# Performance work log

Measured on AMD Instinct MI355X. Metric: run time of the kernel, lower is better.

## Reference

```python
import jax, jax.numpy as jnp
import numpy as np

NC, NG, D = 50000, 3000, 64
E_CG, E_GC, E_GG = 3_000_000, 3_000_000, 100_000
KEEP = 0.9  # 1 - drop_out


def _mask(key, n):
    return (jax.random.uniform(key, (n, 1)) < KEEP).astype(jnp.float32) / KEEP


def setup_inputs() -> dict:
    key = jax.random.key(0)
    ks = jax.random.split(key, 20)
    return {
        "c_feat": jax.random.normal(ks[0], (NC, D), jnp.float32),
        "g_feat": jax.random.normal(ks[1], (NG, D), jnp.float32),
        "cj_cell": jax.random.uniform(ks[2], (NC, 1), jnp.float32),
        "ci_cell": jax.random.uniform(ks[3], (NC, 1), jnp.float32),
        "cj_gene": jax.random.uniform(ks[4], (NG, 1), jnp.float32),
        "ci_gene": jax.random.uniform(ks[5], (NG, 1), jnp.float32),
        "cjj_gene": jax.random.uniform(ks[6], (NG, 1), jnp.float32),
        "cii_gene": jax.random.uniform(ks[7], (NG, 1), jnp.float32),
        "mask_exp": _mask(ks[8], NC),
        "mask_rev": _mask(ks[9], NG),
        "mask_gg": _mask(ks[10], NG),
        "src_cg": jax.random.randint(ks[11], (E_CG,), 0, NC, jnp.int32),
        "dst_cg": jax.random.randint(ks[12], (E_CG,), 0, NG, jnp.int32),
        "src_gc": jax.random.randint(ks[13], (E_GC,), 0, NG, jnp.int32),
        "dst_gc": jax.random.randint(ks[14], (E_GC,), 0, NC, jnp.int32),
        "src_gg": jax.random.randint(ks[15], (E_GG,), 0, NG, jnp.int32),
        "dst_gg": jax.random.randint(ks[16], (E_GG,), 0, NG, jnp.int32),
    }


def _light_conv(src_feats, cj, mask, ci, src, dst, n_dst):
    # weighted_feats = src_feats * dropout(cj); copy_u + sum; scale by ci
    wf = src_feats * (cj * mask)                      # [Nsrc, D]
    agg = jax.ops.segment_sum(wf[src], dst, num_segments=n_dst)  # [Ndst, D]
    return agg * ci


def reference(c_feat, g_feat, cj_cell, ci_cell, cj_gene, ci_gene,
              cjj_gene, cii_gene, mask_exp, mask_rev, mask_gg,
              src_cg, dst_cg, src_gc, dst_gc, src_gg, dst_gg):
    alpha1 = 0.5
    # relation 'exp': cell -> gene
    g_exp = _light_conv(c_feat, cj_cell, mask_exp, ci_gene, src_cg, dst_cg, NG)
    # relation 'reverse-exp': gene -> cell (only relation targeting cells)
    c_out = _light_conv(g_feat, cj_gene, mask_rev, ci_cell, src_gc, dst_gc, NC)
    # relation 'co-exp': gene -> gene (uses cjj/cii)
    g_gg = _light_conv(g_feat, cjj_gene, mask_gg, cii_gene, src_gg, dst_gg, NG)
    # aggregate='stack' over gene dst relations, then alpha-weighted combine
    g_out = alpha1 * g_exp + (1.0 - alpha1) * g_gg
    return (c_out, g_out)
```

## Files before the change

### kernel.cpp

```cpp
#include <hip/hip_runtime.h>

#define NC 50000
#define NG 3000
#define D  64

#define NB_CG 750
#define NB_GC 782
#define PBITS 18
#define TILE  4096
#define NPREP 128
#define CAP   4608
#define GG_CAP 128
#define OVF_CAP 262144

__device__ inline unsigned short f2bf(float x) {
    unsigned u = __float_as_uint(x);
    unsigned r = u + 0x7FFFu + ((u >> 16) & 1u);
    return (unsigned short)(r >> 16);
}

__device__ __forceinline__ void acc8(const uint4& q, float f[8]) {
    f[0] += __uint_as_float(q.x << 16); f[1] += __uint_as_float(q.x & 0xFFFF0000u);
    f[2] += __uint_as_float(q.y << 16); f[3] += __uint_as_float(q.y & 0xFFFF0000u);
    f[4] += __uint_as_float(q.z << 16); f[5] += __uint_as_float(q.z & 0xFFFF0000u);
    f[6] += __uint_as_float(q.w << 16); f[7] += __uint_as_float(q.w & 0xFFFF0000u);
}

__device__ inline void row8f(const float* feat, int s, int l8, float f[8]) {
    const float4* row = (const float4*)(feat + (size_t)s * D);
    const float4 a = row[l8];
    const float4 b = row[l8 + 8];
    f[0] = a.x; f[1] = a.y; f[2] = a.z; f[3] = a.w;
    f[4] = b.x; f[5] = b.y; f[6] = b.z; f[7] = b.w;
}


__global__ __launch_bounds__(256) void partition_kernel(
    const int* __restrict__ src_cg, const int* __restrict__ dst_cg, int e_cg, int nt_cg,
    const int* __restrict__ src_gc, const int* __restrict__ dst_gc, int e_gc, int nt_gc,
    const int* __restrict__ src_gg, const int* __restrict__ dst_gg, int e_gg,
    int* __restrict__ cur_cg, int* __restrict__ cur_gc, int* __restrict__ cnt_gg,
    unsigned* __restrict__ bkt_cg, unsigned* __restrict__ bkt_gc, int* __restrict__ bkt_gg,
    int* __restrict__ ovf_cnt, uint2* __restrict__ ovf,
    const float* __restrict__ cj_cell, const float* __restrict__ mask_exp,
    const float* __restrict__ cj_gene, const float* __restrict__ mask_rev,
    const float* __restrict__ cjj_gene, const float* __restrict__ mask_gg,
    float* __restrict__ w_cell, float* __restrict__ w_rev, float* __restrict__ w_gg,
    const float* __restrict__ c_feat, const float* __restrict__ g_feat,
    unsigned short* __restrict__ wc16, unsigned short* __restrict__ wg16,
    unsigned short* __restrict__ wgg16, int do_cvt)
{
    const int tid = threadIdx.x;
    const int NT2 = nt_cg + nt_gc;

    if (blockIdx.x >= NT2 + 64) {
        const int pb = blockIdx.x - NT2 - 64;
        const long long stride = (long long)NPREP * 256;
        for (long long i = (long long)pb * 256 + tid; i < NC; i += stride)
            w_cell[i] = cj_cell[i] * mask_exp[i];
        for (long long i = (long long)pb * 256 + tid; i < NG; i += stride) {
            w_rev[i] = cj_gene[i] * mask_rev[i];
            w_gg[i]  = cjj_gene[i] * mask_gg[i];
        }
        if (do_cvt) {
            const long long total8 = (long long)(NC + NG) * D / 8;
            for (long long t = (long long)pb * 256 + tid; t < total8; t += stride) {
                const long long base = t * 8;
                if (base < (long long)NC * D) {
                    const int s = (int)(base >> 6);
                    const float w = cj_cell[s] * mask_exp[s];
                    const float4 a = ((const float4*)(c_feat + base))[0];
                    const float4 b = ((const float4*)(c_feat + base))[1];
                    unsigned short* dp = wc16 + base;
                    ((ushort4*)dp)[0] = make_ushort4(f2bf(w*a.x), f2bf(w*a.y), f2bf(w*a.z), f2bf(w*a.w));
                    ((ushort4*)dp)[1] = make_ushort4(f2bf(w*b.x), f2bf(w*b.y), f2bf(w*b.z), f2bf(w*b.w));
                } else {
                    const long long gb = base - (long long)NC * D;
                    const int s = (int)(gb >> 6);
                    const float wr = cj_gene[s] * mask_rev[s];
                    const float wg = cjj_gene[s] * mask_gg[s];
                    const float4 a = ((const float4*)(g_feat + gb))[0];
                    const float4 b = ((const float4*)(g_feat + gb))[1];
                    ((ushort4*)(wg16 + gb))[0]  = make_ushort4(f2bf(wr*a.x), f2bf(wr*a.y), f2bf(wr*a.z), f2bf(wr*a.w));
                    ((ushort4*)(wg16 + gb))[1]  = make_ushort4(f2bf(wr*b.x), f2bf(wr*b.y), f2bf(wr*b.z), f2bf(wr*b.w));
                    ((ushort4*)(wgg16 + gb))[0] = make_ushort4(f2bf(wg*a.x), f2bf(wg*a.y), f2bf(wg*a.z), f2bf(wg*a.w));
                    ((ushort4*)(wgg16 + gb))[1] = make_ushort4(f2bf(wg*b.x), f2bf(wg*b.y), f2bf(wg*b.z), f2bf(wg*b.w));
                }
            }
            if (pb == 0) {
                for (int i = tid; i < D; i += 256) {
                    wc16[(size_t)NC * D + i] = 0;
                    wg16[(size_t)NG * D + i] = 0;
                    wgg16[(size_t)NG * D + i] = 0;
                }
            }
        }
        return;
    }

    if (blockIdx.x >= NT2) {
        for (long long e = (long long)(blockIdx.x - NT2) * 256 + tid; e < e_gg;
             e += (long long)64 * 256) {
            const int dd = dst_gg[e];
            const int ss = src_gg[e];
            if ((unsigned)dd >= (unsigned)NG || (unsigned)ss >= (unsigned)NG) continue;
            const int pos = atomicAdd(&cnt_gg[dd], 1);
            if (pos < GG_CAP) bkt_gg[dd * GG_CAP + pos] = ss;
            else {
                const int op = atomicAdd(ovf_cnt, 1);
                if (op >= 0 && op < OVF_CAP)
                    ovf[op] = make_uint2((2u << 30) | (unsigned)ss, (unsigned)dd);
            }
        }
        return;
    }

    const int* src; const int* dst; int ne; int* cur; unsigned* bkt;
    int shift, nbins, t; unsigned rel;
    if (blockIdx.x < nt_cg) { src = src_cg; dst = dst_cg; ne = e_cg; cur = cur_cg; bkt = bkt_cg; shift = 2; nbins = NB_CG; t = blockIdx.x;         rel = 0u; }
    else                    { src = src_gc; dst = dst_gc; ne = e_gc; cur = cur_gc; bkt = bkt_gc; shift = 6; nbins = NB_GC; t = blockIdx.x - nt_cg; rel = 1u; }
    const long long tb = (long long)t * TILE;
    if (tb >= ne) return;
    const int n = (int)((ne - tb) < TILE ? (ne - tb) : TILE);

    __shared__ int th[784];
    __shared__ int toff[784];
    __shared__ int gs[784];
    __shared__ unsigned staged[TILE];
    const unsigned PMASK = (1u << PBITS) - 1u;
    const unsigned DMASK = (1u << shift) - 1u;

    for (int i = tid; i < nbins; i += 256) th[i] = 0;
    __syncthreads();
    #pragma unroll 4
    for (int k = 0; k < TILE / 256; ++k) {
        int i = k * 256 + tid;
        if (i < n) {
            unsigned b = ((unsigned)dst[tb + i]) >> shift;
            if (b < (unsigned)nbins) atomicAdd(&th[b], 1);
        }
    }
    __syncthreads();
    if (tid < 64) {
        int carry = 0;
        for (int c = 0; c < nbins; c += 64) {
            int idx = c + tid;
            int v = (idx < nbins) ? th[idx] : 0;
            int incl = v;
            #pragma unroll
            for (int d = 1; d < 64; d <<= 1) {
                int x = __shfl_up(incl, d);
                if (tid >= d) incl += x;
            }
            if (idx < nbins) {
                toff[idx] = incl - v + carry;
                gs[idx] = v ? atomicAdd(&cur[idx], v) : 0;
            }
            carry += __shfl(incl, 63);
        }
    }
    __syncthreads();
    #pragma unroll 4
    for (int k = 0; k < TILE / 256; ++k) {
        int i = k * 256 + tid;
        if (i < n) {
            unsigned d = (unsigned)dst[tb + i];
            unsigned s = (unsigned)src[tb + i];
            unsigned b = d >> shift;
            if (b < (unsigned)nbins) {
                int p = atomicAdd(&toff[b], 1);
                if (p >= 0 && p < TILE)
                    staged[p] = (b << PBITS) | (s << shift) | (d & DMASK);
            }
        }
    }
    __syncthreads();
    for (int i = tid; i < n; i += 256) {
        const unsigned v = staged[i];
        const unsigned b = v >> PBITS;
        if (b < (unsigned)nbins) {
            const int orig = toff[b] - th[b];
            const int local = gs[b] + (i - orig);
            if (local >= 0 && local < CAP) {
                bkt[(size_t)b * CAP + local] = v & PMASK;
            } else {
                const unsigned s = (v >> shift) & 0xFFFFu;
                const unsigned dd = (b << shift) | (v & DMASK);
                const int op = atomicAdd(ovf_cnt, 1);
                if (op >= 0 && op < OVF_CAP)
                    ovf[op] = make_uint2((rel << 30) | s, dd);
            }
        }
    }
}


template <bool BF16>
__global__ __launch_bounds__(256, 6) void gather3_kernel(
    const unsigned* __restrict__ bkt_cg, const int* __restrict__ cur_cg,
    const unsigned* __restrict__ bkt_gc, const int* __restrict__ cur_gc,
    const void* __restrict__ fc, const void* __restrict__ fg, const void* __restrict__ fgg,
    const float* __restrict__ craw, const float* __restrict__ graw,
    const float* __restrict__ w_cell, const float* __restrict__ w_rev, const float* __restrict__ w_gg,
    const float* __restrict__ ci_gene, const float* __restrict__ cii_gene, const float* __restrict__ ci_cell,
    const int* __restrict__ cnt_gg, const int* __restrict__ bkt_gg,
    const int* __restrict__ ovf_cnt, const uint2* __restrict__ ovf,
    float* __restrict__ g_out, float* __restrict__ c_out)
{
    __shared__ unsigned short sorted[CAP];
    __shared__ int lh[64];
    __shared__ int loff[64];
    __shared__ int lcur[64];

    const bool is_cg = (blockIdx.x < NB_CG);
    const int bin = is_cg ? blockIdx.x : blockIdx.x - NB_CG;
    int n = (is_cg ? cur_cg : cur_gc)[bin];
    n = n > CAP ? CAP : n;
    const long long base = (long long)bin * CAP;
    const unsigned* bkt = is_cg ? bkt_cg : bkt_gc;
    const void* feat = is_cg ? fc : fg;
    const float* wsrc = is_cg ? w_cell : w_rev;
    const int shift = is_cg ? 2 : 6;
    const int DIVv = is_cg ? 4 : 64;
    const int KPC  = is_cg ? 16 : 1;
    const int DUM  = is_cg ? NC : NG;
    const int tid  = threadIdx.x;
    const int lane = tid & 63;
    const int wid  = tid >> 6;
    const int grp8 = lane >> 3;
    const int l8   = lane & 7;

    for (int i = tid; i < 64; i += 256) { lh[i] = 0; lcur[i] = 0; }
    __syncthreads();
    for (int i = tid; i < n; i += 256) {
        const unsigned v = bkt[base + i];
        const int k = is_cg ? (int)(((v & 3u) << 4) | (((v >> 2) & 0xFFFFu) >> 12))
                            : (int)(v & 63u);
        atomicAdd(&lh[k], 1);
    }
    __syncthreads();
    if (tid < 64) {
        int v = lh[tid];
        int incl = v;
        #pragma unroll
        for (int d = 1; d < 64; d <<= 1) {
            int t = __shfl_up(incl, d);
            if (tid >= d) incl += t;
        }
        loff[tid] = incl - v;
    }
    __syncthreads();
    for (int i = tid; i < n; i += 256) {
        const unsigned v = bkt[base + i];
        const int k = is_cg ? (int)(((v & 3u) << 4) | (((v >> 2) & 0xFFFFu) >> 12))
                            : (int)(v & 63u);
        const int p = loff[k] + atomicAdd(&lcur[k], 1);
        if (p >= 0 && p < CAP) sorted[p] = (unsigned short)((v >> shift) & 0xFFFFu);
    }
    __syncthreads();

    int novf = *ovf_cnt;
    novf = novf < 0 ? 0 : (novf > OVF_CAP ? OVF_CAP : novf);

    for (int cell = wid; cell < DIVv; cell += 4) {
        const int r = (bin << shift) + cell;
        if (r >= (is_cg ? NG : NC)) continue;

        float fA[8] = {0.f, 0.f, 0.f, 0.f, 0.f, 0.f, 0.f, 0.f};
        {
            const int k0 = cell * KPC, k1 = k0 + KPC - 1;
            const int lo = loff[k0], hi = loff[k1] + lh[k1];
            if (BF16) {
                const uint4* fp = (const uint4*)feat;
                for (int jj = lo; jj < hi; jj += 32) {
                    const int b0 = jj + grp8;
                    const int s0 = (b0      < hi) ? (int)sorted[b0]      : DUM;
                    const int s1 = (b0 + 8  < hi) ? (int)sorted[b0 + 8]  : DUM;
                    const int s2 = (b0 + 16 < hi) ? (int)sorted[b0 + 16] : DUM;
                    const int s3 = (b0 + 24 < hi) ? (int)sorted[b0 + 24] : DUM;
                    const uint4 q0 = fp[(size_t)s0 * 8 + l8];
                    const uint4 q1 = fp[(size_t)s1 * 8 + l8];
                    const uint4 q2 = fp[(size_t)s2 * 8 + l8];
                    const uint4 q3 = fp[(size_t)s3 * 8 + l8];
                    acc8(q0, fA); acc8(q1, fA); acc8(q2, fA); acc8(q3, fA);
                }
            } else {
                for (int jj = lo; jj < hi; jj += 8) {
                    const int j = jj + grp8;
                    const bool valid = (j < hi);
                    const int s = valid ? (int)sorted[j] : 0;
                    const float w = valid ? wsrc[s] : 0.0f;
                    float f[8]; row8f((const float*)feat, s, l8, f);
                    #pragma unroll
                    for (int q = 0; q < 8; ++q) fA[q] += w * f[q];
                }
            }
        }

        float fB[8] = {0.f, 0.f, 0.f, 0.f, 0.f, 0.f, 0.f, 0.f};
        if (is_cg) {
            int ngg = cnt_gg[r];
            ngg = ngg > GG_CAP ? GG_CAP : ngg;
            const int* bg = bkt_gg + (size_t)r * GG_CAP;
            if (BF16) {
                const uint4* fp = (const uint4*)fgg;
                for (int jj = 0; jj < ngg; jj += 16) {
                    const int j0 = jj + grp8;
                    const int j1 = jj + 8 + grp8;
                    const int s0 = (j0 < ngg) ? bg[j0] : NG;
                    const int s1 = (j1 < ngg) ? bg[j1] : NG;
                    const uint4 q0 = fp[(size_t)s0 * 8 + l8];
                    const uint4 q1 = fp[(size_t)s1 * 8 + l8];
                    acc8(q0, fB); acc8(q1, fB);
                }
            } else {
                for (int jj = 0; jj < ngg; jj += 8) {
                    const int j = jj + grp8;
                    const bool valid = (j < ngg);
                    const int s = valid ? bg[j] : 0;
                    const float w = valid ? w_gg[s] : 0.0f;
                    float f[8]; row8f(graw, s, l8, f);
                    #pragma unroll
                    for (int q = 0; q < 8; ++q) fB[q] += w * f[q];
                }
            }
        }

        #pragma unroll
        for (int q = 0; q < 8; ++q) {
            #pragma unroll
            for (int off = 8; off < 64; off <<= 1) fA[q] += __shfl_xor(fA[q], off);
        }
        if (is_cg) {
            #pragma unroll
            for (int q = 0; q < 8; ++q) {
                #pragma unroll
                for (int off = 8; off < 64; off <<= 1) fB[q] += __shfl_xor(fB[q], off);
            }
        }

        if (grp8 == 0) {
            float o[8];
            float* outp;
            if (is_cg) {
                const float sa = 0.5f * ci_gene[r];
                const float sb = 0.5f * cii_gene[r];
                outp = g_out + (size_t)r * D;
                #pragma unroll
                for (int q = 0; q < 8; ++q) o[q] = sa * fA[q] + sb * fB[q];
            } else {
                const float sc = ci_cell[r];
                outp = c_out + (size_t)r * D;
                #pragma unroll
                for (int q = 0; q < 8; ++q) o[q] = sc * fA[q];
            }

            if (novf > 0) {
                for (int e = 0; e < novf; ++e) {
                    const uint2 vv = ovf[e];
                    const int d = (int)vv.y;
                    if (d != r) continue;
                    const unsigned relv = vv.x >> 30;
                    const int s = (int)(vv.x & 0x3FFFFFFFu);
                    const float* fr = nullptr; float w = 0.f;
                    if (is_cg) {
                        if (relv == 0u && s < NC)      { fr = craw + (size_t)s * D; w = 0.5f * ci_gene[r] * w_cell[s]; }
                        else if (relv == 2u && s < NG) { fr = graw + (size_t)s * D; w = 0.5f * cii_gene[r] * w_gg[s]; }
                    } else {
                        if (relv == 1u && s < NG)      { fr = graw + (size_t)s * D; w = ci_cell[r] * w_rev[s]; }
                    }
                    if (fr) {
                        #pragma unroll
                        for (int q = 0; q < 8; ++q) {
                            const int elem = BF16 ? (8 * l8 + q)
                                                  : (q < 4 ? 4 * l8 + q : 32 + 4 * l8 + (q - 4));
                            o[q] += w * fr[elem];
                        }
                    }
                }
            }

            if (BF16) {
                *(float4*)(outp + 8 * l8)     = make_float4(o[0], o[1], o[2], o[3]);
                *(float4*)(outp + 8 * l8 + 4) = make_float4(o[4], o[5], o[6], o[7]);
            } else {
                *(float4*)(outp + 4 * l8)      = make_float4(o[0], o[1], o[2], o[3]);
                *(float4*)(outp + 32 + 4 * l8) = make_float4(o[4], o[5], o[6], o[7]);
            }
        }
    }
}


__global__ __launch_bounds__(256) void edge_scatter_kernel(
    const float* __restrict__ feat, const float* __restrict__ cj,
    const float* __restrict__ mask, const float* __restrict__ ci,
    const int* __restrict__ src, const int* __restrict__ dst,
    float* __restrict__ out, int nedges, float alpha)
{
    const int lane16 = threadIdx.x & 15;
    const int eloc   = threadIdx.x >> 4;
    const long long e = (long long)blockIdx.x * 16 + eloc;
    if (e >= nedges) return;
    const int s = src[e];
    const int t = dst[e];
    const float w = cj[s] * mask[s] * ci[t] * alpha;
    const float4 v = *(const float4*)(feat + (size_t)s * D + lane16 * 4);
    float* o = out + (size_t)t * D + lane16 * 4;
#if defined(__HIP_DEVICE_COMPILE__)
    unsafeAtomicAdd(o + 0, w * v.x);
    unsafeAtomicAdd(o + 1, w * v.y);
    unsafeAtomicAdd(o + 2, w * v.z);
    unsafeAtomicAdd(o + 3, w * v.w);
#endif
}


extern "C" void kernel_launch(void* const* d_in, const int* in_sizes, int n_in,
                              void* d_out, int out_size, void* d_ws, size_t ws_size,
                              hipStream_t stream)
{
    const float* c_feat   = (const float*)d_in[0];
    const float* g_feat   = (const float*)d_in[1];
    const float* cj_cell  = (const float*)d_in[2];
    const float* ci_cell  = (const float*)d_in[3];
    const float* cj_gene  = (const float*)d_in[4];
    const float* ci_gene  = (const float*)d_in[5];
    const float* cjj_gene = (const float*)d_in[6];
    const float* cii_gene = (const float*)d_in[7];
    const float* mask_exp = (const float*)d_in[8];
    const float* mask_rev = (const float*)d_in[9];
    const float* mask_gg  = (const float*)d_in[10];
    const int*   src_cg   = (const int*)d_in[11];
    const int*   dst_cg   = (const int*)d_in[12];
    const int*   src_gc   = (const int*)d_in[13];
    const int*   dst_gc   = (const int*)d_in[14];
    const int*   src_gg   = (const int*)d_in[15];
    const int*   dst_gg   = (const int*)d_in[16];

    const int e_cg = in_sizes[11];
    const int e_gc = in_sizes[13];
    const int e_gg = in_sizes[15];

    float* c_out = (float*)d_out;
    float* g_out = (float*)d_out + (size_t)NC * D;

    const int nt_cg = (e_cg + TILE - 1) / TILE;
    const int nt_gc = (e_gc + TILE - 1) / TILE;

    int* ws = (int*)d_ws;
    size_t p = 0;
    int* cur_cg  = ws + p; p += NB_CG;
    int* cur_gc  = ws + p; p += NB_GC;
    int* cnt_gg  = ws + p; p += NG;
    int* ovf_cnt = ws + p; p += 1;
    const size_t zcount = p;
    float* w_cell = (float*)(ws + p); p += NC;
    float* w_rev  = (float*)(ws + p); p += NG;
    float* w_gg   = (float*)(ws + p); p += NG;
    unsigned* bkt_cg = (unsigned*)(ws + p); p += (size_t)NB_CG * CAP;
    unsigned* bkt_gc = (unsigned*)(ws + p); p += (size_t)NB_GC * CAP;
    int* bkt_gg = ws + p; p += (size_t)NG * GG_CAP;
    p = (p + 1) & ~(size_t)1;
    uint2* ovf = (uint2*)(ws + p); p += (size_t)OVF_CAP * 2;
    const size_t need_base = p * sizeof(int);
    p = (p + 3) & ~(size_t)3;
    unsigned short* wc16  = (unsigned short*)(ws + p); p += (size_t)(NC + 1) * D / 2;
    unsigned short* wg16  = (unsigned short*)(ws + p); p += (size_t)(NG + 1) * D / 2;
    unsigned short* wgg16 = (unsigned short*)(ws + p); p += (size_t)(NG + 1) * D / 2;
    const size_t need_full = p * sizeof(int);

    if (need_base > ws_size || e_cg > 3200000 || e_gc > 3200000 || e_gg > 200000) {
        hipMemsetAsync(d_out, 0, (size_t)out_size * sizeof(float), stream);
        edge_scatter_kernel<<<(e_cg + 15) / 16, 256, 0, stream>>>(
            c_feat, cj_cell, mask_exp, ci_gene, src_cg, dst_cg, g_out, e_cg, 0.5f);
        edge_scatter_kernel<<<(e_gc + 15) / 16, 256, 0, stream>>>(
            g_feat, cj_gene, mask_rev, ci_cell, src_gc, dst_gc, c_out, e_gc, 1.0f);
        edge_scatter_kernel<<<(e_gg + 15) / 16, 256, 0, stream>>>(
            g_feat, cjj_gene, mask_gg, cii_gene, src_gg, dst_gg, g_out, e_gg, 0.5f);
        return;
    }
    const int use_bf16 = (need_full <= ws_size) ? 1 : 0;

    hipMemsetAsync(ws, 0, zcount * sizeof(int), stream);

    partition_kernel<<<nt_cg + nt_gc + 64 + NPREP, 256, 0, stream>>>(
        src_cg, dst_cg, e_cg, nt_cg,
        src_gc, dst_gc, e_gc, nt_gc,
        src_gg, dst_gg, e_gg,
        cur_cg, cur_gc, cnt_gg,
        bkt_cg, bkt_gc, bkt_gg,
        ovf_cnt, ovf,
        cj_cell, mask_exp, cj_gene, mask_rev, cjj_gene, mask_gg,
        w_cell, w_rev, w_gg, c_feat, g_feat, wc16, wg16, wgg16, use_bf16);

    if (use_bf16) {
        gather3_kernel<true><<<NB_CG + NB_GC, 256, 0, stream>>>(
            bkt_cg, cur_cg, bkt_gc, cur_gc,
            (const void*)wc16, (const void*)wg16, (const void*)wgg16,
            c_feat, g_feat,
            w_cell, w_rev, w_gg, ci_gene, cii_gene, ci_cell,
            cnt_gg, bkt_gg, ovf_cnt, ovf, g_out, c_out);
    } else {
        gather3_kernel<false><<<NB_CG + NB_GC, 256, 0, stream>>>(
            bkt_cg, cur_cg, bkt_gc, cur_gc,
            (const void*)c_feat, (const void*)g_feat, (const void*)g_feat,
            c_feat, g_feat,
            w_cell, w_rev, w_gg, ci_gene, cii_gene, ci_cell,
            cnt_gg, bkt_gg, ovf_cnt, ovf, g_out, c_out);
    }
}
```

Baseline: 268.9 us.

## Replace tiled radix partition with direct per-destination atomic bucket fill

```diff
diff --git a/kernel.cpp b/kernel.cpp
--- a/kernel.cpp
+++ b/kernel.cpp
@@ -4,14 +4,13 @@
 #define NG 3000
 #define D  64
 
-#define NB_CG 750
-#define NB_GC 782
-#define PBITS 18
-#define TILE  4096
+#define SBCG 8
+#define CAPCG 176
+#define CAPGC 96
+#define GG_CAP 128
+#define OVF_CAP 65536
+#define NFILL 1920
 #define NPREP 128
-#define CAP   4608
-#define GG_CAP 128
-#define OVF_CAP 262144
 
 __device__ inline unsigned short f2bf(float x) {
     unsigned u = __float_as_uint(x);
@@ -26,21 +25,14 @@
     f[6] += __uint_as_float(q.w << 16); f[7] += __uint_as_float(q.w & 0xFFFF0000u);
 }
 
-__device__ inline void row8f(const float* feat, int s, int l8, float f[8]) {
-    const float4* row = (const float4*)(feat + (size_t)s * D);
-    const float4 a = row[l8];
-    const float4 b = row[l8 + 8];
-    f[0] = a.x; f[1] = a.y; f[2] = a.z; f[3] = a.w;
-    f[4] = b.x; f[5] = b.y; f[6] = b.z; f[7] = b.w;
-}
-
-
-__global__ __launch_bounds__(256) void partition_kernel(
-    const int* __restrict__ src_cg, const int* __restrict__ dst_cg, int e_cg, int nt_cg,
-    const int* __restrict__ src_gc, const int* __restrict__ dst_gc, int e_gc, int nt_gc,
+
+__global__ __launch_bounds__(256) void fill_kernel(
+    const int* __restrict__ src_cg, const int* __restrict__ dst_cg, int e_cg,
+    const int* __restrict__ src_gc, const int* __restrict__ dst_gc, int e_gc,
     const int* __restrict__ src_gg, const int* __restrict__ dst_gg, int e_gg,
-    int* __restrict__ cur_cg, int* __restrict__ cur_gc, int* __restrict__ cnt_gg,
-    unsigned* __restrict__ bkt_cg, unsigned* __restrict__ bkt_gc, int* __restrict__ bkt_gg,
+    int* __restrict__ cnt_cg2, int* __restrict__ cnt_gc, int* __restrict__ cnt_gg,
+    unsigned short* __restrict__ bkt_cg, unsigned short* __restrict__ bkt_gc,
+    int* __restrict__ bkt_gg,
     int* __restrict__ ovf_cnt, uint2* __restrict__ ovf,
     const float* __restrict__ cj_cell, const float* __restrict__ mask_exp,
     const float* __restrict__ cj_gene, const float* __restrict__ mask_rev,
@@ -48,13 +40,12 @@
     float* __restrict__ w_cell, float* __restrict__ w_rev, float* __restrict__ w_gg,
     const float* __restrict__ c_feat, const float* __restrict__ g_feat,
     unsigned short* __restrict__ wc16, unsigned short* __restrict__ wg16,
-    unsigned short* __restrict__ wgg16, int do_cvt)
+    unsigned short* __restrict__ wgg16)
 {
     const int tid = threadIdx.x;
-    const int NT2 = nt_cg + nt_gc;
-
-    if (blockIdx.x >= NT2 + 64) {
-        const int pb = blockIdx.x - NT2 - 64;
+
+    if (blockIdx.x >= NFILL) {
+        const int pb = blockIdx.x - NFILL;
         const long long stride = (long long)NPREP * 256;
         for (long long i = (long long)pb * 256 + tid; i < NC; i += stride)
             w_cell[i] = cj_cell[i] * mask_exp[i];
@@ -62,267 +53,142 @@
             w_rev[i] = cj_gene[i] * mask_rev[i];
             w_gg[i]  = cjj_gene[i] * mask_gg[i];
         }
-        if (do_cvt) {
-            const long long total8 = (long long)(NC + NG) * D / 8;
-            for (long long t = (long long)pb * 256 + tid; t < total8; t += stride) {
-                const long long base = t * 8;
-                if (base < (long long)NC * D) {
-                    const int s = (int)(base >> 6);
-                    const float w = cj_cell[s] * mask_exp[s];
-                    const float4 a = ((const float4*)(c_feat + base))[0];
-                    const float4 b = ((const float4*)(c_feat + base))[1];
-                    unsigned short* dp = wc16 + base;
-                    ((ushort4*)dp)[0] = make_ushort4(f2bf(w*a.x), f2bf(w*a.y), f2bf(w*a.z), f2bf(w*a.w));
-                    ((ushort4*)dp)[1] = make_ushort4(f2bf(w*b.x), f2bf(w*b.y), f2bf(w*b.z), f2bf(w*b.w));
-                } else {
-                    const long long gb = base - (long long)NC * D;
-                    const int s = (int)(gb >> 6);
-                    const float wr = cj_gene[s] * mask_rev[s];
-                    const float wg = cjj_gene[s] * mask_gg[s];
-                    const float4 a = ((const float4*)(g_feat + gb))[0];
-                    const float4 b = ((const float4*)(g_feat + gb))[1];
-                    ((ushort4*)(wg16 + gb))[0]  = make_ushort4(f2bf(wr*a.x), f2bf(wr*a.y), f2bf(wr*a.z), f2bf(wr*a.w));
-                    ((ushort4*)(wg16 + gb))[1]  = make_ushort4(f2bf(wr*b.x), f2bf(wr*b.y), f2bf(wr*b.z), f2bf(wr*b.w));
-                    ((ushort4*)(wgg16 + gb))[0] = make_ushort4(f2bf(wg*a.x), f2bf(wg*a.y), f2bf(wg*a.z), f2bf(wg*a.w));
-                    ((ushort4*)(wgg16 + gb))[1] = make_ushort4(f2bf(wg*b.x), f2bf(wg*b.y), f2bf(wg*b.z), f2bf(wg*b.w));
-                }
-            }
-            if (pb == 0) {
-                for (int i = tid; i < D; i += 256) {
-                    wc16[(size_t)NC * D + i] = 0;
-                    wg16[(size_t)NG * D + i] = 0;
-                    wgg16[(size_t)NG * D + i] = 0;
-                }
+        const long long total8 = (long long)(NC + NG) * D / 8;
+        for (long long t = (long long)pb * 256 + tid; t < total8; t += stride) {
+            const long long base = t * 8;
+            if (base < (long long)NC * D) {
+                const int s = (int)(base >> 6);
+                const float w = cj_cell[s] * mask_exp[s];
+                const float4 a = ((const float4*)(c_feat + base))[0];
+                const float4 b = ((const float4*)(c_feat + base))[1];
+                unsigned short* dp = wc16 + base;
+                ((ushort4*)dp)[0] = make_ushort4(f2bf(w*a.x), f2bf(w*a.y), f2bf(w*a.z), f2bf(w*a.w));
+                ((ushort4*)dp)[1] = make_ushort4(f2bf(w*b.x), f2bf(w*b.y), f2bf(w*b.z), f2bf(w*b.w));
+            } else {
+                const long long gb = base - (long long)NC * D;
+                const int s = (int)(gb >> 6);
+                const float wr = cj_gene[s] * mask_rev[s];
+                const float wg = cjj_gene[s] * mask_gg[s];
+                const float4 a = ((const float4*)(g_feat + gb))[0];
+                const float4 b = ((const float4*)(g_feat + gb))[1];
+                ((ushort4*)(wg16 + gb))[0]  = make_ushort4(f2bf(wr*a.x), f2bf(wr*a.y), f2bf(wr*a.z), f2bf(wr*a.w));
+                ((ushort4*)(wg16 + gb))[1]  = make_ushort4(f2bf(wr*b.x), f2bf(wr*b.y), f2bf(wr*b.z), f2bf(wr*b.w));
+                ((ushort4*)(wgg16 + gb))[0] = make_ushort4(f2bf(wg*a.x), f2bf(wg*a.y), f2bf(wg*a.z), f2bf(wg*a.w));
+                ((ushort4*)(wgg16 + gb))[1] = make_ushort4(f2bf(wg*b.x), f2bf(wg*b.y), f2bf(wg*b.z), f2bf(wg*b.w));
+            }
+        }
+        if (pb == 0) {
+            for (int i = tid; i < D; i += 256) {
+                wc16[(size_t)NC * D + i] = 0;
+                wg16[(size_t)NG * D + i] = 0;
+                wgg16[(size_t)NG * D + i] = 0;
             }
         }
         return;
     }
 
-    if (blockIdx.x >= NT2) {
-        for (long long e = (long long)(blockIdx.x - NT2) * 256 + tid; e < e_gg;
-             e += (long long)64 * 256) {
-            const int dd = dst_gg[e];
-            const int ss = src_gg[e];
-            if ((unsigned)dd >= (unsigned)NG || (unsigned)ss >= (unsigned)NG) continue;
-            const int pos = atomicAdd(&cnt_gg[dd], 1);
-            if (pos < GG_CAP) bkt_gg[dd * GG_CAP + pos] = ss;
+    const long long stride = (long long)NFILL * 256;
+    const long long e0 = (long long)blockIdx.x * 256 + tid;
+
+    for (long long e = e0; e < e_cg; e += stride) {
+        const int d = dst_cg[e], s = src_cg[e];
+        if ((unsigned)d < (unsigned)NG && (unsigned)s < (unsigned)NC) {
+            const int k = d * SBCG + (s & (SBCG - 1));
+            const int pos = atomicAdd(&cnt_cg2[k], 1);
+            if (pos < CAPCG) bkt_cg[(size_t)k * CAPCG + pos] = (unsigned short)s;
             else {
                 const int op = atomicAdd(ovf_cnt, 1);
                 if (op >= 0 && op < OVF_CAP)
-                    ovf[op] = make_uint2((2u << 30) | (unsigned)ss, (unsigned)dd);
-            }
-        }
-        return;
-    }
-
-    const int* src; const int* dst; int ne; int* cur; unsigned* bkt;
-    int shift, nbins, t; unsigned rel;
-    if (blockIdx.x < nt_cg) { src = src_cg; dst = dst_cg; ne = e_cg; cur = cur_cg; bkt = bkt_cg; shift = 2; nbins = NB_CG; t = blockIdx.x;         rel = 0u; }
-    else                    { src = src_gc; dst = dst_gc; ne = e_gc; cur = cur_gc; bkt = bkt_gc; shift = 6; nbins = NB_GC; t = blockIdx.x - nt_cg; rel = 1u; }
-    const long long tb = (long long)t * TILE;
-    if (tb >= ne) return;
-    const int n = (int)((ne - tb) < TILE ? (ne - tb) : TILE);
-
-    __shared__ int th[784];
-    __shared__ int toff[784];
-    __shared__ int gs[784];
-    __shared__ unsigned staged[TILE];
-    const unsigned PMASK = (1u << PBITS) - 1u;
-    const unsigned DMASK = (1u << shift) - 1u;
-
-    for (int i = tid; i < nbins; i += 256) th[i] = 0;
-    __syncthreads();
-    #pragma unroll 4
-    for (int k = 0; k < TILE / 256; ++k) {
-        int i = k * 256 + tid;
-        if (i < n) {
-            unsigned b = ((unsigned)dst[tb + i]) >> shift;
-            if (b < (unsigned)nbins) atomicAdd(&th[b], 1);
-        }
-    }
-    __syncthreads();
-    if (tid < 64) {
-        int carry = 0;
-        for (int c = 0; c < nbins; c += 64) {
-            int idx = c + tid;
-            int v = (idx < nbins) ? th[idx] : 0;
-            int incl = v;
-            #pragma unroll
-            for (int d = 1; d < 64; d <<= 1) {
-                int x = __shfl_up(incl, d);
-                if (tid >= d) incl += x;
-            }
-            if (idx < nbins) {
-                toff[idx] = incl - v + carry;
-                gs[idx] = v ? atomicAdd(&cur[idx], v) : 0;
-            }
-            carry += __shfl(incl, 63);
-        }
-    }
-    __syncthreads();
-    #pragma unroll 4
-    for (int k = 0; k < TILE / 256; ++k) {
-        int i = k * 256 + tid;
-        if (i < n) {
-            unsigned d = (unsigned)dst[tb + i];
-            unsigned s = (unsigned)src[tb + i];
-            unsigned b = d >> shift;
-            if (b < (unsigned)nbins) {
-                int p = atomicAdd(&toff[b], 1);
-                if (p >= 0 && p < TILE)
-                    staged[p] = (b << PBITS) | (s << shift) | (d & DMASK);
-            }
-        }
-    }
-    __syncthreads();
-    for (int i = tid; i < n; i += 256) {
-        const unsigned v = staged[i];
-        const unsigned b = v >> PBITS;
-        if (b < (unsigned)nbins) {
-            const int orig = toff[b] - th[b];
-            const int local = gs[b] + (i - orig);
-            if (local >= 0 && local < CAP) {
-                bkt[(size_t)b * CAP + local] = v & PMASK;
-            } else {
-                const unsigned s = (v >> shift) & 0xFFFFu;
-                const unsigned dd = (b << shift) | (v & DMASK);
+                    ovf[op] = make_uint2((0u << 30) | (unsigned)s, (unsigned)d);
+            }
+        }
+    }
+    for (long long e = e0; e < e_gc; e += stride) {
+        const int d = dst_gc[e], s = src_gc[e];
+        if ((unsigned)d < (unsigned)NC && (unsigned)s < (unsigned)NG) {
+            const int pos = atomicAdd(&cnt_gc[d], 1);
+            if (pos < CAPGC) bkt_gc[(size_t)d * CAPGC + pos] = (unsigned short)s;
+            else {
                 const int op = atomicAdd(ovf_cnt, 1);
                 if (op >= 0 && op < OVF_CAP)
-                    ovf[op] = make_uint2((rel << 30) | s, dd);
-            }
-        }
-    }
-}
-
-
-template <bool BF16>
-__global__ __launch_bounds__(256, 6) void gather3_kernel(
-    const unsigned* __restrict__ bkt_cg, const int* __restrict__ cur_cg,
-    const unsigned* __restrict__ bkt_gc, const int* __restrict__ cur_gc,
-    const void* __restrict__ fc, const void* __restrict__ fg, const void* __restrict__ fgg,
+                    ovf[op] = make_uint2((1u << 30) | (unsigned)s, (unsigned)d);
+            }
+        }
+    }
+    for (long long e = e0; e < e_gg; e += stride) {
+        const int d = dst_gg[e], s = src_gg[e];
+        if ((unsigned)d < (unsigned)NG && (unsigned)s < (unsigned)NG) {
+            const int pos = atomicAdd(&cnt_gg[d], 1);
+            if (pos < GG_CAP) bkt_gg[(size_t)d * GG_CAP + pos] = s;
+            else {
+                const int op = atomicAdd(ovf_cnt, 1);
+                if (op >= 0 && op < OVF_CAP)
+                    ovf[op] = make_uint2((2u << 30) | (unsigned)s, (unsigned)d);
+            }
+        }
+    }
+}
+
+
+__global__ __launch_bounds__(256, 8) void gather_kernel(
+    const int* __restrict__ cnt_cg2, const unsigned short* __restrict__ bkt_cg,
+    const int* __restrict__ cnt_gc, const unsigned short* __restrict__ bkt_gc,
+    const int* __restrict__ cnt_gg, const int* __restrict__ bkt_gg,
+    const uint4* __restrict__ wc, const uint4* __restrict__ wg, const uint4* __restrict__ wgg,
     const float* __restrict__ craw, const float* __restrict__ graw,
     const float* __restrict__ w_cell, const float* __restrict__ w_rev, const float* __restrict__ w_gg,
     const float* __restrict__ ci_gene, const float* __restrict__ cii_gene, const float* __restrict__ ci_cell,
-    const int* __restrict__ cnt_gg, const int* __restrict__ bkt_gg,
     const int* __restrict__ ovf_cnt, const uint2* __restrict__ ovf,
     float* __restrict__ g_out, float* __restrict__ c_out)
 {
-    __shared__ unsigned short sorted[CAP];
-    __shared__ int lh[64];
-    __shared__ int loff[64];
-    __shared__ int lcur[64];
-
-    const bool is_cg = (blockIdx.x < NB_CG);
-    const int bin = is_cg ? blockIdx.x : blockIdx.x - NB_CG;
-    int n = (is_cg ? cur_cg : cur_gc)[bin];
-    n = n > CAP ? CAP : n;
-    const long long base = (long long)bin * CAP;
-    const unsigned* bkt = is_cg ? bkt_cg : bkt_gc;
-    const void* feat = is_cg ? fc : fg;
-    const float* wsrc = is_cg ? w_cell : w_rev;
-    const int shift = is_cg ? 2 : 6;
-    const int DIVv = is_cg ? 4 : 64;
-    const int KPC  = is_cg ? 16 : 1;
-    const int DUM  = is_cg ? NC : NG;
+    __shared__ float part[5][64];
+
     const int tid  = threadIdx.x;
     const int lane = tid & 63;
     const int wid  = tid >> 6;
     const int grp8 = lane >> 3;
     const int l8   = lane & 7;
 
-    for (int i = tid; i < 64; i += 256) { lh[i] = 0; lcur[i] = 0; }
-    __syncthreads();
-    for (int i = tid; i < n; i += 256) {
-        const unsigned v = bkt[base + i];
-        const int k = is_cg ? (int)(((v & 3u) << 4) | (((v >> 2) & 0xFFFFu) >> 12))
-                            : (int)(v & 63u);
-        atomicAdd(&lh[k], 1);
-    }
-    __syncthreads();
-    if (tid < 64) {
-        int v = lh[tid];
-        int incl = v;
-        #pragma unroll
-        for (int d = 1; d < 64; d <<= 1) {
-            int t = __shfl_up(incl, d);
-            if (tid >= d) incl += t;
-        }
-        loff[tid] = incl - v;
-    }
-    __syncthreads();
-    for (int i = tid; i < n; i += 256) {
-        const unsigned v = bkt[base + i];
-        const int k = is_cg ? (int)(((v & 3u) << 4) | (((v >> 2) & 0xFFFFu) >> 12))
-                            : (int)(v & 63u);
-        const int p = loff[k] + atomicAdd(&lcur[k], 1);
-        if (p >= 0 && p < CAP) sorted[p] = (unsigned short)((v >> shift) & 0xFFFFu);
-    }
-    __syncthreads();
-
     int novf = *ovf_cnt;
     novf = novf < 0 ? 0 : (novf > OVF_CAP ? OVF_CAP : novf);
 
-    for (int cell = wid; cell < DIVv; cell += 4) {
-        const int r = (bin << shift) + cell;
-        if (r >= (is_cg ? NG : NC)) continue;
+    if (blockIdx.x < NG) {
+        const int g = blockIdx.x;
 
         float fA[8] = {0.f, 0.f, 0.f, 0.f, 0.f, 0.f, 0.f, 0.f};
-        {
-            const int k0 = cell * KPC, k1 = k0 + KPC - 1;
-            const int lo = loff[k0], hi = loff[k1] + lh[k1];
-            if (BF16) {
-                const uint4* fp = (const uint4*)feat;
-                for (int jj = lo; jj < hi; jj += 32) {
-                    const int b0 = jj + grp8;
-                    const int s0 = (b0      < hi) ? (int)sorted[b0]      : DUM;
-                    const int s1 = (b0 + 8  < hi) ? (int)sorted[b0 + 8]  : DUM;
-                    const int s2 = (b0 + 16 < hi) ? (int)sorted[b0 + 16] : DUM;
-                    const int s3 = (b0 + 24 < hi) ? (int)sorted[b0 + 24] : DUM;
-                    const uint4 q0 = fp[(size_t)s0 * 8 + l8];
-                    const uint4 q1 = fp[(size_t)s1 * 8 + l8];
-                    const uint4 q2 = fp[(size_t)s2 * 8 + l8];
-                    const uint4 q3 = fp[(size_t)s3 * 8 + l8];
-                    acc8(q0, fA); acc8(q1, fA); acc8(q2, fA); acc8(q3, fA);
-                }
-            } else {
-                for (int jj = lo; jj < hi; jj += 8) {
-                    const int j = jj + grp8;
-                    const bool valid = (j < hi);
-                    const int s = valid ? (int)sorted[j] : 0;
-                    const float w = valid ? wsrc[s] : 0.0f;
-                    float f[8]; row8f((const float*)feat, s, l8, f);
-                    #pragma unroll
-                    for (int q = 0; q < 8; ++q) fA[q] += w * f[q];
-                }
+        #pragma unroll
+        for (int t = 0; t < 2; ++t) {
+            const int k = g * SBCG + wid + 4 * t;
+            int n = cnt_cg2[k];
+            n = n > CAPCG ? CAPCG : n;
+            const unsigned short* bp = bkt_cg + (size_t)k * CAPCG;
+            for (int jj = 0; jj < n; jj += 32) {
+                const int b0 = jj + grp8;
+                const int s0 = (b0      < n) ? (int)bp[b0]      : NC;
+                const int s1 = (b0 + 8  < n) ? (int)bp[b0 + 8]  : NC;
+                const int s2 = (b0 + 16 < n) ? (int)bp[b0 + 16] : NC;
+                const int s3 = (b0 + 24 < n) ? (int)bp[b0 + 24] : NC;
+                const uint4 q0 = wc[(size_t)s0 * 8 + l8];
+                const uint4 q1 = wc[(size_t)s1 * 8 + l8];
+                const uint4 q2 = wc[(size_t)s2 * 8 + l8];
+                const uint4 q3 = wc[(size_t)s3 * 8 + l8];
+                acc8(q0, fA); acc8(q1, fA); acc8(q2, fA); acc8(q3, fA);
             }
         }
 
         float fB[8] = {0.f, 0.f, 0.f, 0.f, 0.f, 0.f, 0.f, 0.f};
-        if (is_cg) {
-            int ngg = cnt_gg[r];
-            ngg = ngg > GG_CAP ? GG_CAP : ngg;
-            const int* bg = bkt_gg + (size_t)r * GG_CAP;
-            if (BF16) {
-                const uint4* fp = (const uint4*)fgg;
-                for (int jj = 0; jj < ngg; jj += 16) {
-                    const int j0 = jj + grp8;
-                    const int j1 = jj + 8 + grp8;
-                    const int s0 = (j0 < ngg) ? bg[j0] : NG;
-                    const int s1 = (j1 < ngg) ? bg[j1] : NG;
-                    const uint4 q0 = fp[(size_t)s0 * 8 + l8];
-                    const uint4 q1 = fp[(size_t)s1 * 8 + l8];
-                    acc8(q0, fB); acc8(q1, fB);
-                }
-            } else {
-                for (int jj = 0; jj < ngg; jj += 8) {
-                    const int j = jj + grp8;
-                    const bool valid = (j < ngg);
-                    const int s = valid ? bg[j] : 0;
-                    const float w = valid ? w_gg[s] : 0.0f;
-                    float f[8]; row8f(graw, s, l8, f);
-                    #pragma unroll
-                    for (int q = 0; q < 8; ++q) fB[q] += w * f[q];
-                }
+        if (wid == 0) {
+            int n = cnt_gg[g];
+            n = n > GG_CAP ? GG_CAP : n;
+            const int* bp = bkt_gg + (size_t)g * GG_CAP;
+            for (int jj = 0; jj < n; jj += 16) {
+                const int j0 = jj + grp8;
+                const int j1 = jj + 8 + grp8;
+                const int s0 = (j0 < n) ? bp[j0] : NG;
+                const int s1 = (j1 < n) ? bp[j1] : NG;
+                const uint4 q0 = wgg[(size_t)s0 * 8 + l8];
+                const uint4 q1 = wgg[(size_t)s1 * 8 + l8];
+                acc8(q0, fB); acc8(q1, fB);
             }
         }
 
@@ -331,62 +197,94 @@
             #pragma unroll
             for (int off = 8; off < 64; off <<= 1) fA[q] += __shfl_xor(fA[q], off);
         }
-        if (is_cg) {
+        if (wid == 0) {
             #pragma unroll
             for (int q = 0; q < 8; ++q) {
                 #pragma unroll
                 for (int off = 8; off < 64; off <<= 1) fB[q] += __shfl_xor(fB[q], off);
             }
         }
-
         if (grp8 == 0) {
-            float o[8];
-            float* outp;
-            if (is_cg) {
-                const float sa = 0.5f * ci_gene[r];
-                const float sb = 0.5f * cii_gene[r];
-                outp = g_out + (size_t)r * D;
+            #pragma unroll
+            for (int q = 0; q < 8; ++q) part[wid][8 * l8 + q] = fA[q];
+            if (wid == 0) {
                 #pragma unroll
-                for (int q = 0; q < 8; ++q) o[q] = sa * fA[q] + sb * fB[q];
-            } else {
-                const float sc = ci_cell[r];
-                outp = c_out + (size_t)r * D;
-                #pragma unroll
-                for (int q = 0; q < 8; ++q) o[q] = sc * fA[q];
-            }
-
+                for (int q = 0; q < 8; ++q) part[4][8 * l8 + q] = fB[q];
+            }
+        }
+        __syncthreads();
+
+        if (tid < 64) {
+            const float v = part[0][tid] + part[1][tid] + part[2][tid] + part[3][tid];
+            float o = 0.5f * ci_gene[g] * v + 0.5f * cii_gene[g] * part[4][tid];
             if (novf > 0) {
                 for (int e = 0; e < novf; ++e) {
                     const uint2 vv = ovf[e];
-                    const int d = (int)vv.y;
-                    if (d != r) continue;
+                    if ((int)vv.y != g) continue;
                     const unsigned relv = vv.x >> 30;
                     const int s = (int)(vv.x & 0x3FFFFFFFu);
-                    const float* fr = nullptr; float w = 0.f;
-                    if (is_cg) {
-                        if (relv == 0u && s < NC)      { fr = craw + (size_t)s * D; w = 0.5f * ci_gene[r] * w_cell[s]; }
-                        else if (relv == 2u && s < NG) { fr = graw + (size_t)s * D; w = 0.5f * cii_gene[r] * w_gg[s]; }
-                    } else {
-                        if (relv == 1u && s < NG)      { fr = graw + (size_t)s * D; w = ci_cell[r] * w_rev[s]; }
-                    }
-                    if (fr) {
+                    if (relv == 0u && s < NC)
+                        o += 0.5f * ci_gene[g] * w_cell[s] * craw[(size_t)s * D + tid];
+                    else if (relv == 2u && s < NG)
+                        o += 0.5f * cii_gene[g] * w_gg[s] * graw[(size_t)s * D + tid];
+                }
+            }
+            g_out[(size_t)g * D + tid] = o;
+        }
+        return;
+    }
+
+    const int r0 = (blockIdx.x - NG) * 16;
+    #pragma unroll
+    for (int t = 0; t < 4; ++t) {
+        const int r = r0 + wid * 4 + t;
+        if (r >= NC) continue;
+        int n = cnt_gc[r];
+        n = n > CAPGC ? CAPGC : n;
+        const unsigned short* bp = bkt_gc + (size_t)r * CAPGC;
+
+        float fA[8] = {0.f, 0.f, 0.f, 0.f, 0.f, 0.f, 0.f, 0.f};
+        for (int jj = 0; jj < n; jj += 32) {
+            const int b0 = jj + grp8;
+            const int s0 = (b0      < n) ? (int)bp[b0]      : NG;
+            const int s1 = (b0 + 8  < n) ? (int)bp[b0 + 8]  : NG;
+            const int s2 = (b0 + 16 < n) ? (int)bp[b0 + 16] : NG;
+            const int s3 = (b0 + 24 < n) ? (int)bp[b0 + 24] : NG;
+            const uint4 q0 = wg[(size_t)s0 * 8 + l8];
+            const uint4 q1 = wg[(size_t)s1 * 8 + l8];
+            const uint4 q2 = wg[(size_t)s2 * 8 + l8];
+            const uint4 q3 = wg[(size_t)s3 * 8 + l8];
+            acc8(q0, fA); acc8(q1, fA); acc8(q2, fA); acc8(q3, fA);
+        }
+
+        #pragma unroll
+        for (int q = 0; q < 8; ++q) {
+            #pragma unroll
+            for (int off = 8; off < 64; off <<= 1) fA[q] += __shfl_xor(fA[q], off);
+        }
+
+        if (grp8 == 0) {
+            const float sc = ci_cell[r];
+            float o[8];
+            #pragma unroll
+            for (int q = 0; q < 8; ++q) o[q] = sc * fA[q];
+            if (novf > 0) {
+                for (int e = 0; e < novf; ++e) {
+                    const uint2 vv = ovf[e];
+                    if ((int)vv.y != r) continue;
+                    const unsigned relv = vv.x >> 30;
+                    const int s = (int)(vv.x & 0x3FFFFFFFu);
+                    if (relv == 1u && s < NG) {
+                        const float w = sc * w_rev[s];
                         #pragma unroll
-                        for (int q = 0; q < 8; ++q) {
-                            const int elem = BF16 ? (8 * l8 + q)
-                                                  : (q < 4 ? 4 * l8 + q : 32 + 4 * l8 + (q - 4));
-                            o[q] += w * fr[elem];
-                        }
+                        for (int q = 0; q < 8; ++q)
+                            o[q] += w * graw[(size_t)s * D + 8 * l8 + q];
                     }
                 }
             }
-
-            if (BF16) {
-                *(float4*)(outp + 8 * l8)     = make_float4(o[0], o[1], o[2], o[3]);
-                *(float4*)(outp + 8 * l8 + 4) = make_float4(o[4], o[5], o[6], o[7]);
-            } else {
-                *(float4*)(outp + 4 * l8)      = make_float4(o[0], o[1], o[2], o[3]);
-                *(float4*)(outp + 32 + 4 * l8) = make_float4(o[4], o[5], o[6], o[7]);
-            }
+            float* outp = c_out + (size_t)r * D;
+            *(float4*)(outp + 8 * l8)     = make_float4(o[0], o[1], o[2], o[3]);
+            *(float4*)(outp + 8 * l8 + 4) = make_float4(o[4], o[5], o[6], o[7]);
         }
     }
 }
@@ -445,32 +343,28 @@
     float* c_out = (float*)d_out;
     float* g_out = (float*)d_out + (size_t)NC * D;
 
-    const int nt_cg = (e_cg + TILE - 1) / TILE;
-    const int nt_gc = (e_gc + TILE - 1) / TILE;
-
     int* ws = (int*)d_ws;
     size_t p = 0;
-    int* cur_cg  = ws + p; p += NB_CG;
-    int* cur_gc  = ws + p; p += NB_GC;
+    int* cnt_cg2 = ws + p; p += (size_t)NG * SBCG;
+    int* cnt_gc  = ws + p; p += NC;
     int* cnt_gg  = ws + p; p += NG;
     int* ovf_cnt = ws + p; p += 1;
     const size_t zcount = p;
     float* w_cell = (float*)(ws + p); p += NC;
     float* w_rev  = (float*)(ws + p); p += NG;
     float* w_gg   = (float*)(ws + p); p += NG;
-    unsigned* bkt_cg = (unsigned*)(ws + p); p += (size_t)NB_CG * CAP;
-    unsigned* bkt_gc = (unsigned*)(ws + p); p += (size_t)NB_GC * CAP;
+    unsigned short* bkt_cg = (unsigned short*)(ws + p); p += ((size_t)NG * SBCG * CAPCG + 1) / 2;
+    unsigned short* bkt_gc = (unsigned short*)(ws + p); p += ((size_t)NC * CAPGC + 1) / 2;
     int* bkt_gg = ws + p; p += (size_t)NG * GG_CAP;
     p = (p + 1) & ~(size_t)1;
     uint2* ovf = (uint2*)(ws + p); p += (size_t)OVF_CAP * 2;
-    const size_t need_base = p * sizeof(int);
     p = (p + 3) & ~(size_t)3;
     unsigned short* wc16  = (unsigned short*)(ws + p); p += (size_t)(NC + 1) * D / 2;
     unsigned short* wg16  = (unsigned short*)(ws + p); p += (size_t)(NG + 1) * D / 2;
     unsigned short* wgg16 = (unsigned short*)(ws + p); p += (size_t)(NG + 1) * D / 2;
-    const size_t need_full = p * sizeof(int);
-
-    if (need_base > ws_size || e_cg > 3200000 || e_gc > 3200000 || e_gg > 200000) {
+    const size_t need = p * sizeof(int);
+
+    if (need > ws_size || e_cg > 3200000 || e_gc > 3200000 || e_gg > 200000) {
         hipMemsetAsync(d_out, 0, (size_t)out_size * sizeof(float), stream);
         edge_scatter_kernel<<<(e_cg + 15) / 16, 256, 0, stream>>>(
             c_feat, cj_cell, mask_exp, ci_gene, src_cg, dst_cg, g_out, e_cg, 0.5f);
@@ -480,33 +374,20 @@
             g_feat, cjj_gene, mask_gg, cii_gene, src_gg, dst_gg, g_out, e_gg, 0.5f);
         return;
     }
-    const int use_bf16 = (need_full <= ws_size) ? 1 : 0;
 
     hipMemsetAsync(ws, 0, zcount * sizeof(int), stream);
 
-    partition_kernel<<<nt_cg + nt_gc + 64 + NPREP, 256, 0, stream>>>(
-        src_cg, dst_cg, e_cg, nt_cg,
-        src_gc, dst_gc, e_gc, nt_gc,
-        src_gg, dst_gg, e_gg,
-        cur_cg, cur_gc, cnt_gg,
-        bkt_cg, bkt_gc, bkt_gg,
-        ovf_cnt, ovf,
+    fill_kernel<<<NFILL + NPREP, 256, 0, stream>>>(
+        src_cg, dst_cg, e_cg, src_gc, dst_gc, e_gc, src_gg, dst_gg, e_gg,
+        cnt_cg2, cnt_gc, cnt_gg, bkt_cg, bkt_gc, bkt_gg, ovf_cnt, ovf,
         cj_cell, mask_exp, cj_gene, mask_rev, cjj_gene, mask_gg,
-        w_cell, w_rev, w_gg, c_feat, g_feat, wc16, wg16, wgg16, use_bf16);
-
-    if (use_bf16) {
-        gather3_kernel<true><<<NB_CG + NB_GC, 256, 0, stream>>>(
-            bkt_cg, cur_cg, bkt_gc, cur_gc,
-            (const void*)wc16, (const void*)wg16, (const void*)wgg16,
-            c_feat, g_feat,
-            w_cell, w_rev, w_gg, ci_gene, cii_gene, ci_cell,
-            cnt_gg, bkt_gg, ovf_cnt, ovf, g_out, c_out);
-    } else {
-        gather3_kernel<false><<<NB_CG + NB_GC, 256, 0, stream>>>(
-            bkt_cg, cur_cg, bkt_gc, cur_gc,
-            (const void*)c_feat, (const void*)g_feat, (const void*)g_feat,
-            c_feat, g_feat,
-            w_cell, w_rev, w_gg, ci_gene, cii_gene, ci_cell,
-            cnt_gg, bkt_gg, ovf_cnt, ovf, g_out, c_out);
-    }
-}
+        w_cell, w_rev, w_gg, c_feat, g_feat, wc16, wg16, wgg16);
+
+    const int ngather = NG + (NC + 15) / 16;
+    gather_kernel<<<ngather, 256, 0, stream>>>(
+        cnt_cg2, bkt_cg, cnt_gc, bkt_gc, cnt_gg, bkt_gg,
+        (const uint4*)wc16, (const uint4*)wg16, (const uint4*)wgg16,
+        c_feat, g_feat,
+        w_cell, w_rev, w_gg, ci_gene, cii_gene, ci_cell,
+        ovf_cnt, ovf, g_out, c_out);
+}
```

Measured after the change: 647.1 us. 141% more time.
